# Kernel tuning notes

Measured on AMD Instinct MI355X. Metric: run time of the kernel, lower is better.

The kernel has to match this reference:

```python
import jax, jax.numpy as jnp
import numpy as np

C = 256          # channels
K = 7            # involution kernel size
GC = 16          # group_channels (fixed in source)
G = C // GC      # groups = 16
RED = C // 4     # reduction channels = 64
B, H, W = 4, 56, 56


def setup_inputs() -> dict:
    key = jax.random.key(0)
    k0, k1, k2 = jax.random.split(key, 3)
    x = jax.random.normal(k0, (B, C, H, W), jnp.float32)
    w1 = jax.random.normal(k1, (RED, C), jnp.float32) * (1.0 / np.sqrt(C))
    b1 = jnp.zeros((RED,), jnp.float32)
    w2 = jax.random.normal(k2, (K * K * G, RED), jnp.float32) * (1.0 / np.sqrt(RED))
    b2 = jnp.zeros((K * K * G,), jnp.float32)
    return {"x": x, "w1": w1, "b1": b1, "w2": w2, "b2": b2}


def reference(x, w1, b1, w2, b2):
    b, c, h, w = x.shape
    # 1x1 conv generator: conv1 (C -> C/4) + ReLU, conv2 (C/4 -> K^2*G)
    t = jax.nn.relu(jnp.einsum('bchw,oc->bohw', x, w1) + b1[None, :, None, None])
    weight = jnp.einsum('bohw,ko->bkhw', t, w2) + b2[None, :, None, None]
    weight = weight.reshape(b, G, K * K, h, w)             # (b, G, K^2, h, w)
    # unfold: patches ordered (C, kh, kw) channel-slowest, matching torch.nn.Unfold
    pad = (K - 1) // 2
    patches = jax.lax.conv_general_dilated_patches(
        x, (K, K), (1, 1), [(pad, pad), (pad, pad)],
        dimension_numbers=('NCHW', 'OIHW', 'NCHW'))        # (b, C*K*K, h, w)
    patches = patches.reshape(b, G, GC, K * K, h, w)
    # per-pixel, per-group weighted sum over the K^2 window positions
    out = jnp.einsum('bgkhw,bgckhw->bgchw', weight, patches)
    return out.reshape(b, c, h, w)
```

## Files before the change

kernel.cpp:

```cpp
#include <hip/hip_runtime.h>

#define B_    4
#define C_    256
#define Kk    7
#define GC_   16
#define G_    16
#define RED_  64
#define H_    56
#define W_    56
#define HW_   3136
#define KK_   49
#define KG_   784
#define NP_   12544

typedef float  f4    __attribute__((ext_vector_type(4)));
typedef float  f32x4 __attribute__((ext_vector_type(4)));
typedef __bf16 bf16x8 __attribute__((ext_vector_type(8)));
typedef __bf16 bf16x4 __attribute__((ext_vector_type(4)));
typedef unsigned short u16;
typedef u16    u16x4 __attribute__((ext_vector_type(4)));

__device__ __forceinline__ f4 ld4(const float* p) { return *(const f4*)p; }
__device__ __forceinline__ void st4(float* p, f4 v) { *(f4*)p = v; }
__device__ __forceinline__ float bf2f(u16 u) {
    return __uint_as_float(((unsigned)u) << 16);
}
__device__ __forceinline__ bf16x8 pack8(f4 lo, f4 hi) {
    bf16x8 r;
    r[0] = (__bf16)lo[0]; r[1] = (__bf16)lo[1]; r[2] = (__bf16)lo[2]; r[3] = (__bf16)lo[3];
    r[4] = (__bf16)hi[0]; r[5] = (__bf16)hi[1]; r[6] = (__bf16)hi[2]; r[7] = (__bf16)hi[3];
    return r;
}

__global__ __launch_bounds__(256) void xt_kernel(const float* __restrict__ x,
                                                 __bf16* __restrict__ xt) {
    __shared__ __bf16 lt[64][68];
    const int tid = threadIdx.x;
    const int P0  = blockIdx.x * 64;
    const int c0  = blockIdx.y * 64;
    const int b   = P0 / HW_;
    const int p0  = P0 - b * HW_;

    const int pq  = tid & 15;
    const int crb = tid >> 4;
#pragma unroll
    for (int i = 0; i < 4; ++i) {
        const int cr = crb + i * 16;
        const f4 v = ld4(x + (size_t)(b * C_ + c0 + cr) * HW_ + p0 + pq * 4);
#pragma unroll
        for (int j = 0; j < 4; ++j) lt[pq * 4 + j][cr] = (__bf16)v[j];
    }
    __syncthreads();
    const int cq  = tid & 15;
    const int plb = tid >> 4;
#pragma unroll
    for (int i = 0; i < 4; ++i) {
        const int pl = plb + i * 16;
        const bf16x4 rv = *(const bf16x4*)&lt[pl][cq * 4];
        *(bf16x4*)(xt + (size_t)(P0 + pl) * C_ + c0 + cq * 4) = rv;
    }
}

__global__ __launch_bounds__(256) void gen1m(const __bf16* __restrict__ xt,
                                             const float* __restrict__ w1,
                                             const float* __restrict__ b1,
                                             __bf16* __restrict__ t) {
    const int lane = threadIdx.x & 63;
    const int wave = threadIdx.x >> 6;
    const int row  = lane & 15;
    const int kg   = lane >> 4;
    const int P0   = blockIdx.x * 256 + wave * 64;

    f32x4 acc[4][4];
#pragma unroll
    for (int m = 0; m < 4; ++m)
#pragma unroll
        for (int c = 0; c < 4; ++c) acc[m][c] = f32x4(0.f);

#pragma unroll
    for (int ks = 0; ks < 8; ++ks) {
        bf16x8 af[4], bf[4];
#pragma unroll
        for (int mt = 0; mt < 4; ++mt) {
            const float* wr = w1 + (size_t)(mt * 16 + row) * C_ + ks * 32 + kg * 8;
            af[mt] = pack8(ld4(wr), ld4(wr + 4));
        }
#pragma unroll
        for (int cg = 0; cg < 4; ++cg)
            bf[cg] = *(const bf16x8*)(xt + (size_t)(P0 + cg * 16 + row) * C_
                                         + ks * 32 + kg * 8);
#pragma unroll
        for (int mt = 0; mt < 4; ++mt)
#pragma unroll
            for (int cg = 0; cg < 4; ++cg)
                acc[mt][cg] = __builtin_amdgcn_mfma_f32_16x16x32_bf16(
                    af[mt], bf[cg], acc[mt][cg], 0, 0, 0);
    }

#pragma unroll
    for (int mt = 0; mt < 4; ++mt) {
        const f4 bias = ld4(b1 + mt * 16 + kg * 4);
#pragma unroll
        for (int cg = 0; cg < 4; ++cg) {
            bf16x4 pk;
#pragma unroll
            for (int j = 0; j < 4; ++j)
                pk[j] = (__bf16)fmaxf(acc[mt][cg][j] + bias[j], 0.f);
            *(bf16x4*)(t + (size_t)(P0 + cg * 16 + row) * RED_ + mt * 16 + kg * 4) = pk;
        }
    }
}

__global__ __launch_bounds__(256) void gen2_mfma(const __bf16* __restrict__ t,
                                                 const float* __restrict__ w2,
                                                 const float* __restrict__ b2,
                                                 __bf16* __restrict__ wgt) {
    const int lane = threadIdx.x & 63;
    const int wave = threadIdx.x >> 6;
    const int row  = lane & 15;
    const int kg   = lane >> 4;
    const int P0   = blockIdx.x * 256 + wave * 64;
    const int k0   = blockIdx.y * 64;
    const int nMt  = (blockIdx.y == 12) ? 1 : 4;

    bf16x8 bfrag[4][2];
#pragma unroll
    for (int cg = 0; cg < 4; ++cg)
#pragma unroll
        for (int ks = 0; ks < 2; ++ks)
            bfrag[cg][ks] = *(const bf16x8*)(t + (size_t)(P0 + cg * 16 + row) * RED_
                                               + ks * 32 + kg * 8);

    for (int mt = 0; mt < nMt; ++mt) {
        const int kr = k0 + mt * 16 + row;
        const float* w2r = w2 + (size_t)kr * RED_ + kg * 8;
        const bf16x8 afr0 = pack8(ld4(w2r),      ld4(w2r + 4));
        const bf16x8 afr1 = pack8(ld4(w2r + 32), ld4(w2r + 36));
        f32x4 acc[4] = {f32x4(0.f), f32x4(0.f), f32x4(0.f), f32x4(0.f)};
#pragma unroll
        for (int cg = 0; cg < 4; ++cg) {
            acc[cg] = __builtin_amdgcn_mfma_f32_16x16x32_bf16(afr0, bfrag[cg][0], acc[cg], 0, 0, 0);
            acc[cg] = __builtin_amdgcn_mfma_f32_16x16x32_bf16(afr1, bfrag[cg][1], acc[cg], 0, 0, 0);
        }
        const f4 bias = ld4(b2 + k0 + mt * 16 + kg * 4);
#pragma unroll
        for (int cg = 0; cg < 4; ++cg) {
            const int Pcg = P0 + cg * 16;
            const int b   = Pcg / HW_;
            const int p   = Pcg - b * HW_ + row;
            const size_t base = ((size_t)b * KG_ + (size_t)(k0 + mt * 16 + kg * 4)) * HW_ + p;
#pragma unroll
            for (int j = 0; j < 4; ++j)
                wgt[base + (size_t)j * HW_] = (__bf16)(acc[cg][j] + bias[j]);
        }
    }
}

#define BR_  4
#define XR_  10
#define XST_ 68
__global__ __launch_bounds__(256) void inv_kernel(const float* __restrict__ x,
                                                  const u16* __restrict__ wgt,
                                                  float* __restrict__ out) {
    __shared__ float xs[GC_][XR_][XST_];
    __shared__ u16   wsm[KK_][BR_][W_];
    const int tid = threadIdx.x;
    const int r0  = blockIdx.x * BR_;
    const int g   = blockIdx.y;
    const int b   = blockIdx.z;

    for (int idx = tid; idx < GC_ * XR_ * 16; idx += 256) {
        const int c   = idx / (XR_ * 16);
        const int rem = idx - c * (XR_ * 16);
        const int hr  = rem >> 4;
        const int wq  = rem & 15;
        const int h   = r0 - 3 + hr;
        f4 v = {0.f, 0.f, 0.f, 0.f};
        if (h >= 0 && h < H_) {
            const float* xr_ = x + (size_t)(b * C_ + g * GC_ + c) * HW_ + h * W_;
            const int w0 = wq * 4 - 3;
            if (wq >= 1 && wq <= 13) {
                v = ld4(xr_ + w0);
            } else {
#pragma unroll
                for (int j = 0; j < 4; ++j) {
                    const int w = w0 + j;
                    if (w >= 0 && w < W_) v[j] = xr_[w];
                }
            }
        }
        *(f4*)&xs[c][hr][wq * 4] = v;
    }
    for (int idx = tid; idx < KK_ * BR_ * 14; idx += 256) {
        const int k   = idx / (BR_ * 14);
        const int rem = idx - k * (BR_ * 14);
        const int r   = rem / 14;
        const int cq  = rem - r * 14;
        const u16x4 v = *(const u16x4*)(wgt + ((size_t)b * KG_ + (size_t)g * KK_ + k) * HW_
                                            + (r0 + r) * W_ + cq * 4);
        *(u16x4*)&wsm[k][r][cq * 4] = v;
    }
    __syncthreads();

    if (tid >= 224) return;
    const int cq  = tid % 14;
    const int r   = (tid / 14) & 3;
    const int cg4 = tid / 56;

    f4 acc[4] = {f4(0.f), f4(0.f), f4(0.f), f4(0.f)};
#pragma unroll
    for (int kh = 0; kh < Kk; ++kh) {
        float tf[7][4];
#pragma unroll
        for (int kw = 0; kw < 7; ++kw) {
            const u16x4 tv = *(const u16x4*)&wsm[kh * 7 + kw][r][cq * 4];
#pragma unroll
            for (int j = 0; j < 4; ++j) tf[kw][j] = bf2f(tv[j]);
        }
        const int hr = r + kh;
#pragma unroll
        for (int ci = 0; ci < 4; ++ci) {
            const float* xrow = &xs[cg4 * 4 + ci][hr][cq * 4];
            const f4 x0 = ld4(xrow), x1 = ld4(xrow + 4), x2 = ld4(xrow + 8);
            float xw[12];
#pragma unroll
            for (int j = 0; j < 4; ++j) { xw[j] = x0[j]; xw[4 + j] = x1[j]; xw[8 + j] = x2[j]; }
#pragma unroll
            for (int kw = 0; kw < 7; ++kw)
#pragma unroll
                for (int j = 0; j < 4; ++j)
                    acc[ci][j] = fmaf(tf[kw][j], xw[j + kw], acc[ci][j]);
        }
    }

#pragma unroll
    for (int ci = 0; ci < 4; ++ci)
        st4(out + (size_t)(b * C_ + g * GC_ + cg4 * 4 + ci) * HW_ + (r0 + r) * W_ + cq * 4,
            acc[ci]);
}

extern "C" void kernel_launch(void* const* d_in, const int* in_sizes, int n_in,
                              void* d_out, int out_size, void* d_ws, size_t ws_size,
                              hipStream_t stream) {
    const float* x  = (const float*)d_in[0];
    const float* w1 = (const float*)d_in[1];
    const float* b1 = (const float*)d_in[2];
    const float* w2 = (const float*)d_in[3];
    const float* b2 = (const float*)d_in[4];
    float* out = (float*)d_out;

    char* ws = (char*)d_ws;
    __bf16* xt  = (__bf16*)ws;
    __bf16* t   = (__bf16*)(ws + (size_t)NP_ * C_ * 2);
    __bf16* wgt = (__bf16*)(ws + (size_t)NP_ * C_ * 2 + (size_t)NP_ * RED_ * 2);

    xt_kernel <<<dim3(NP_ / 64, C_ / 64), 256, 0, stream>>>(x, xt);
    gen1m     <<<dim3(NP_ / 256),         256, 0, stream>>>(xt, w1, b1, t);
    gen2_mfma <<<dim3(NP_ / 256, 13),     256, 0, stream>>>(t, w2, b2, wgt);
    inv_kernel<<<dim3(14, G_, B_),        256, 0, stream>>>(x, (const u16*)wgt, out);
}
```

Measured before the change: 133.8 us.

## Stage bf16 generator weights in LDS and shrink gen1 tiles per block

Both generator GEMM kernels now convert their fp32 weight matrices (w1, w2) to bf16 once per block into shared memory. Previously every wave reloaded and packed them from global memory, and the MFMA A-fragments are now read from LDS. gen1 also drops from 64 pixels per wave to 16, launching four times as many blocks to improve occupancy and parallelism. The cost is a block-wide barrier plus a redundant per-block conversion of the full w1 matrix, which is now repeated across many more blocks.

```diff
diff --git a/kernel.cpp b/kernel.cpp
--- a/kernel.cpp
+++ b/kernel.cpp
@@ -25,12 +25,6 @@
 __device__ __forceinline__ float bf2f(u16 u) {
     return __uint_as_float(((unsigned)u) << 16);
 }
-__device__ __forceinline__ bf16x8 pack8(f4 lo, f4 hi) {
-    bf16x8 r;
-    r[0] = (__bf16)lo[0]; r[1] = (__bf16)lo[1]; r[2] = (__bf16)lo[2]; r[3] = (__bf16)lo[3];
-    r[4] = (__bf16)hi[0]; r[5] = (__bf16)hi[1]; r[6] = (__bf16)hi[2]; r[7] = (__bf16)hi[3];
-    return r;
-}
 
 __global__ __launch_bounds__(256) void xt_kernel(const float* __restrict__ x,
                                                  __bf16* __restrict__ xt) {
@@ -61,62 +55,64 @@
     }
 }
 
-__global__ __launch_bounds__(256) void gen1m(const __bf16* __restrict__ xt,
-                                             const float* __restrict__ w1,
-                                             const float* __restrict__ b1,
-                                             __bf16* __restrict__ t) {
-    const int lane = threadIdx.x & 63;
-    const int wave = threadIdx.x >> 6;
+__global__ __launch_bounds__(256) void gen1m2(const __bf16* __restrict__ xt,
+                                              const float* __restrict__ w1,
+                                              const float* __restrict__ b1,
+                                              __bf16* __restrict__ t) {
+    __shared__ __bf16 w1s[64][260];
+    const int tid  = threadIdx.x;
+    const int lane = tid & 63;
+    const int wave = tid >> 6;
     const int row  = lane & 15;
     const int kg   = lane >> 4;
-    const int P0   = blockIdx.x * 256 + wave * 64;
-
-    f32x4 acc[4][4];
-#pragma unroll
-    for (int m = 0; m < 4; ++m)
-#pragma unroll
-        for (int c = 0; c < 4; ++c) acc[m][c] = f32x4(0.f);
-
-#pragma unroll
-    for (int ks = 0; ks < 8; ++ks) {
-        bf16x8 af[4], bf[4];
+    const int P0w  = blockIdx.x * 64 + wave * 16;
+
+    const __bf16* bp = xt + (size_t)(P0w + row) * C_ + kg * 8;
+    bf16x8 bv[8];
+#pragma unroll
+    for (int ks = 0; ks < 8; ++ks) bv[ks] = *(const bf16x8*)(bp + ks * 32);
+
+#pragma unroll
+    for (int i = 0; i < 16; ++i) {
+        const int q  = tid + i * 256;
+        const int r  = q >> 6;
+        const int c0 = (q & 63) * 4;
+        const f4 v = ld4(w1 + (size_t)r * C_ + c0);
+        bf16x4 pk;
+#pragma unroll
+        for (int j = 0; j < 4; ++j) pk[j] = (__bf16)v[j];
+        *(bf16x4*)&w1s[r][c0] = pk;
+    }
+    __syncthreads();
+
+    f32x4 acc[4] = {f32x4(0.f), f32x4(0.f), f32x4(0.f), f32x4(0.f)};
+#pragma unroll
+    for (int ks = 0; ks < 8; ++ks)
 #pragma unroll
         for (int mt = 0; mt < 4; ++mt) {
-            const float* wr = w1 + (size_t)(mt * 16 + row) * C_ + ks * 32 + kg * 8;
-            af[mt] = pack8(ld4(wr), ld4(wr + 4));
-        }
-#pragma unroll
-        for (int cg = 0; cg < 4; ++cg)
-            bf[cg] = *(const bf16x8*)(xt + (size_t)(P0 + cg * 16 + row) * C_
-                                         + ks * 32 + kg * 8);
-#pragma unroll
-        for (int mt = 0; mt < 4; ++mt)
-#pragma unroll
-            for (int cg = 0; cg < 4; ++cg)
-                acc[mt][cg] = __builtin_amdgcn_mfma_f32_16x16x32_bf16(
-                    af[mt], bf[cg], acc[mt][cg], 0, 0, 0);
-    }
+            const bf16x8 af = *(const bf16x8*)&w1s[mt * 16 + row][ks * 32 + kg * 8];
+            acc[mt] = __builtin_amdgcn_mfma_f32_16x16x32_bf16(af, bv[ks], acc[mt], 0, 0, 0);
+        }
 
 #pragma unroll
     for (int mt = 0; mt < 4; ++mt) {
         const f4 bias = ld4(b1 + mt * 16 + kg * 4);
-#pragma unroll
-        for (int cg = 0; cg < 4; ++cg) {
-            bf16x4 pk;
-#pragma unroll
-            for (int j = 0; j < 4; ++j)
-                pk[j] = (__bf16)fmaxf(acc[mt][cg][j] + bias[j], 0.f);
-            *(bf16x4*)(t + (size_t)(P0 + cg * 16 + row) * RED_ + mt * 16 + kg * 4) = pk;
-        }
-    }
-}
-
-__global__ __launch_bounds__(256) void gen2_mfma(const __bf16* __restrict__ t,
-                                                 const float* __restrict__ w2,
-                                                 const float* __restrict__ b2,
-                                                 __bf16* __restrict__ wgt) {
-    const int lane = threadIdx.x & 63;
-    const int wave = threadIdx.x >> 6;
+        bf16x4 pk;
+#pragma unroll
+        for (int j = 0; j < 4; ++j)
+            pk[j] = (__bf16)fmaxf(acc[mt][j] + bias[j], 0.f);
+        *(bf16x4*)(t + (size_t)(P0w + row) * RED_ + mt * 16 + kg * 4) = pk;
+    }
+}
+
+__global__ __launch_bounds__(256) void gen2_mfma2(const __bf16* __restrict__ t,
+                                                  const float* __restrict__ w2,
+                                                  const float* __restrict__ b2,
+                                                  __bf16* __restrict__ wgt) {
+    __shared__ __bf16 w2s[64][68];
+    const int tid  = threadIdx.x;
+    const int lane = tid & 63;
+    const int wave = tid >> 6;
     const int row  = lane & 15;
     const int kg   = lane >> 4;
     const int P0   = blockIdx.x * 256 + wave * 64;
@@ -131,11 +127,23 @@
             bfrag[cg][ks] = *(const bf16x8*)(t + (size_t)(P0 + cg * 16 + row) * RED_
                                                + ks * 32 + kg * 8);
 
+#pragma unroll
+    for (int i = 0; i < 4; ++i) {
+        const int q  = tid + i * 256;
+        const int r  = q >> 4;
+        const int c0 = (q & 15) * 4;
+        f4 v = {0.f, 0.f, 0.f, 0.f};
+        if (k0 + r < KG_) v = ld4(w2 + (size_t)(k0 + r) * RED_ + c0);
+        bf16x4 pk;
+#pragma unroll
+        for (int j = 0; j < 4; ++j) pk[j] = (__bf16)v[j];
+        *(bf16x4*)&w2s[r][c0] = pk;
+    }
+    __syncthreads();
+
     for (int mt = 0; mt < nMt; ++mt) {
-        const int kr = k0 + mt * 16 + row;
-        const float* w2r = w2 + (size_t)kr * RED_ + kg * 8;
-        const bf16x8 afr0 = pack8(ld4(w2r),      ld4(w2r + 4));
-        const bf16x8 afr1 = pack8(ld4(w2r + 32), ld4(w2r + 36));
+        const bf16x8 afr0 = *(const bf16x8*)&w2s[mt * 16 + row][kg * 8];
+        const bf16x8 afr1 = *(const bf16x8*)&w2s[mt * 16 + row][32 + kg * 8];
         f32x4 acc[4] = {f32x4(0.f), f32x4(0.f), f32x4(0.f), f32x4(0.f)};
 #pragma unroll
         for (int cg = 0; cg < 4; ++cg) {
@@ -254,8 +262,8 @@
     __bf16* t   = (__bf16*)(ws + (size_t)NP_ * C_ * 2);
     __bf16* wgt = (__bf16*)(ws + (size_t)NP_ * C_ * 2 + (size_t)NP_ * RED_ * 2);
 
-    xt_kernel <<<dim3(NP_ / 64, C_ / 64), 256, 0, stream>>>(x, xt);
-    gen1m     <<<dim3(NP_ / 256),         256, 0, stream>>>(xt, w1, b1, t);
-    gen2_mfma <<<dim3(NP_ / 256, 13),     256, 0, stream>>>(t, w2, b2, wgt);
-    inv_kernel<<<dim3(14, G_, B_),        256, 0, stream>>>(x, (const u16*)wgt, out);
-}
+    xt_kernel  <<<dim3(NP_ / 64, C_ / 64), 256, 0, stream>>>(x, xt);
+    gen1m2     <<<dim3(NP_ / 64),          256, 0, stream>>>(xt, w1, b1, t);
+    gen2_mfma2 <<<dim3(NP_ / 256, 13),     256, 0, stream>>>(t, w2, b2, wgt);
+    inv_kernel <<<dim3(14, G_, B_),        256, 0, stream>>>(x, (const u16*)wgt, out);
+}
```

Result: faster. 121.5 us (-9.2%).
